# Kernel optimization log

Hardware: AMD Instinct MI355X
Metric: run time of the kernel (lower is better)

## Reference

```python
import jax, jax.numpy as jnp
import numpy as np

N = 100000
MUL = 16


def _build_cg():
    # Real-basis Clebsch-Gordan (Wigner-3j-style) coefficients, shape (2l1+1, 2l2+1, 2lo+1),
    # each normalized to unit Frobenius norm per output component (e3nn component normalization).
    eps = np.zeros((3, 3, 3), np.float32)
    for a, b, c in [(0, 1, 2), (1, 2, 0), (2, 0, 1)]:
        eps[a, b, c] = 1.0
        eps[a, c, b] = -1.0
    s2 = np.float32(1.0 / np.sqrt(2.0))
    q = np.zeros((5, 3, 3), np.float32)  # l=2 real harmonics: xy, yz, 3z^2-r^2, xz, x^2-y^2
    q[0, 0, 1] = q[0, 1, 0] = s2
    q[1, 1, 2] = q[1, 2, 1] = s2
    q[2] = np.diag([-1.0, -1.0, 2.0]).astype(np.float32) / np.sqrt(6.0)
    q[3, 0, 2] = q[3, 2, 0] = s2
    q[4] = np.diag([1.0, -1.0, 0.0]).astype(np.float32) * s2
    cg000 = jnp.ones((1, 1, 1), jnp.float32)                                   # 0e x 0e -> 0e
    cg011 = jnp.asarray(np.eye(3, dtype=np.float32)[None])                      # 0e x 1o -> 1o
    cg110 = jnp.asarray((np.eye(3, dtype=np.float32) / np.sqrt(3.0))[:, :, None])  # 1o x 1o -> 0e
    cg111 = jnp.asarray(eps * s2)                                               # 1o x 1o -> 1e
    cg112 = jnp.asarray(np.transpose(q, (1, 2, 0)))                             # 1o x 1o -> 2e
    return cg000, cg011, cg110, cg111, cg112


def _path(x1, x2, cg, w, alpha):
    # 'uvw' tensor-product path: out[z,w,m] = alpha * sum_{u,v,i,j} x1[z,u,i] x2[z,v,j] cg[i,j,m] w[u,v,w]
    # Contraction order chosen to keep the largest intermediate at [z,u,w,j].
    t = jnp.einsum('zvj,uvw->zuwj', x2, w)
    s = jnp.einsum('zui,zuwj->zwij', x1, t)
    return alpha * jnp.einsum('zwij,ijm->zwm', s, cg)


def _tensor_square(x, w0, w1, w2, w3, w4):
    n = x.shape[0]
    x0 = x[:, :MUL].reshape(n, MUL, 1)       # 16x0e
    x1 = x[:, MUL:].reshape(n, MUL, 3)       # 16x1o
    cg000, cg011, cg110, cg111, cg112 = _build_cg()
    a2 = 1.0 / np.sqrt(MUL * MUL * 2.0)      # 0e output receives 2 paths
    a1 = 1.0 / np.sqrt(MUL * MUL * 1.0)
    o_0e = _path(x0, x0, cg000, w0, a2) + _path(x1, x1, cg110, w2, a2)
    o_1o = _path(x0, x1, cg011, w1, a1)
    o_1e = _path(x1, x1, cg111, w3, a1)
    o_2e = _path(x1, x1, cg112, w4, a1)
    return jnp.concatenate([o.reshape(n, -1) for o in (o_0e, o_1o, o_1e, o_2e)], axis=1)


def setup_inputs() -> dict:
    key = jax.random.key(0)
    kx, k0, k1, k2, k3, k4 = jax.random.split(key, 6)
    return {
        'x': jax.random.normal(kx, (N, MUL * 1 + MUL * 3), jnp.float32),
        'w0': jax.random.normal(k0, (MUL, MUL, MUL), jnp.float32),
        'w1': jax.random.normal(k1, (MUL, MUL, MUL), jnp.float32),
        'w2': jax.random.normal(k2, (MUL, MUL, MUL), jnp.float32),
        'w3': jax.random.normal(k3, (MUL, MUL, MUL), jnp.float32),
        'w4': jax.random.normal(k4, (MUL, MUL, MUL), jnp.float32),
    }


def reference(x, w0, w1, w2, w3, w4):
    return _tensor_square(x, w0, w1, w2, w3, w4)
```

## Files before the change

### kernel.cpp

```cpp
#include <hip/hip_runtime.h>
#include <hip/hip_bf16.h>

typedef __attribute__((ext_vector_type(8))) short short8;
typedef __attribute__((ext_vector_type(4))) float float4v;
typedef __attribute__((ext_vector_type(4))) int int4v;

#define S_A 0.04419417382415922f
#define S_B 0.025515518153991442f
#define S_C 0.0625f

static __device__ __forceinline__ unsigned short f2bfu(float f) {
    __hip_bfloat16 h = __float2bfloat16(f);
    return __builtin_bit_cast(unsigned short, h);
}

static __device__ __forceinline__ unsigned pack_bf2(float a, float b) {
    return ((unsigned)f2bfu(b) << 16) | (unsigned)f2bfu(a);
}

__global__ __launch_bounds__(256, 2)
void tsq_kernel(const float* __restrict__ x,
                const float* __restrict__ wA,
                const float* __restrict__ wB,
                const float* __restrict__ wC,
                const float* __restrict__ wD,
                const float* __restrict__ wE,
                float* __restrict__ out,
                int nrows)
{
    __shared__ __attribute__((aligned(16))) unsigned short wlds[5 * 8 * 64 * 8];
    __shared__ __attribute__((aligned(16))) float xlds[64 * 68];

    const int tid = threadIdx.x;

    #pragma unroll
    for (int p = 0; p < 5; p++) {
        const float* wp = (p == 0) ? wA : (p == 1) ? wB : (p == 2) ? wC : (p == 3) ? wD : wE;
        for (int rem = tid; rem < 4096; rem += 256) {
            int k = rem >> 4;
            int w = rem & 15;
            int c = k >> 5, kk = k & 31;
            int lane = ((kk >> 3) << 4) | w;
            int j = kk & 7;
            wlds[(((p * 8 + c) * 64 + lane) << 3) | j] = f2bfu(wp[rem]);
        }
    }

    {
        const long long rowbase = (long long)blockIdx.x * 64;
        const float* xg = x + rowbase * 64;
        #pragma unroll
        for (int q = 0; q < 4; q++) {
            int f = q * 1024 + tid * 4;
            int row = f >> 6, col = f & 63;
            float4v v = {0.f, 0.f, 0.f, 0.f};
            if (rowbase + row < nrows) v = *(const float4v*)(xg + f);
            *(float4v*)&xlds[row * 68 + col] = v;
        }
    }
    __syncthreads();

    const int wave = tid >> 6;
    const int l = tid & 63;
    const long long z0 = (long long)blockIdx.x * 64 + wave * 16;
    if (z0 >= nrows) return;

    const int r  = l & 15;
    const int g  = l >> 4;
    const int v0 = (g & 1) * 8;
    const int uo = g >> 1;
    const float* xr = &xlds[(wave * 16 + r) * 68];

    float av[8], bx[8], byv[8], bzv[8];
    #pragma unroll
    for (int j = 0; j < 8; j++) {
        av[j]  = xr[v0 + j];
        bx[j]  = xr[16 + (v0 + j) * 3 + 0];
        byv[j] = xr[16 + (v0 + j) * 3 + 1];
        bzv[j] = xr[16 + (v0 + j) * 3 + 2];
    }

    float4v acc[13];
    #pragma unroll
    for (int m = 0; m < 13; m++) acc[m] = (float4v){0.f, 0.f, 0.f, 0.f};

    constexpr int pm[13] = {0, 1, 2, 2, 2, 3, 3, 3, 4, 4, 4, 4, 4};

    #pragma unroll
    for (int c = 0; c < 8; c++) {
        const int u = c * 2 + uo;
        const float u0 = xr[u];
        const float ux = xr[16 + u * 3 + 0];
        const float uy = xr[16 + u * 3 + 1];
        const float uz = xr[16 + u * 3 + 2];

        int4v fri[13];
        #pragma unroll
        for (int t = 0; t < 4; t++) {
            float bva[13], bvb[13];
            auto build = [&](int j, float* bv) {
                const float A0 = av[j], X = bx[j], Y = byv[j], Z = bzv[j];
                const float p00 = ux * X, p01 = ux * Y, p02 = ux * Z;
                const float p10 = uy * X, p11 = uy * Y, p12 = uy * Z;
                const float p20 = uz * X, p21 = uz * Y, p22 = uz * Z;
                bv[0]  = u0 * A0;
                bv[1]  = p00 + p11 + p22;
                bv[2]  = u0 * X;
                bv[3]  = u0 * Y;
                bv[4]  = u0 * Z;
                bv[5]  = p12 - p21;
                bv[6]  = p20 - p02;
                bv[7]  = p01 - p10;
                bv[8]  = p01 + p10;
                bv[9]  = p12 + p21;
                bv[10] = 2.0f * p22 - p00 - p11;
                bv[11] = p02 + p20;
                bv[12] = p00 - p11;
            };
            build(2 * t, bva);
            build(2 * t + 1, bvb);
            #pragma unroll
            for (int m = 0; m < 13; m++) fri[m][t] = (int)pack_bf2(bva[m], bvb[m]);
        }

        short8 wf[5];
        #pragma unroll
        for (int p = 0; p < 5; p++)
            wf[p] = *(const short8*)&wlds[(((p * 8 + c) * 64 + l) << 3)];

        #pragma unroll
        for (int m = 0; m < 13; m++) {
            short8 frm = __builtin_bit_cast(short8, fri[m]);
            acc[m] = __builtin_amdgcn_mfma_f32_16x16x32_bf16(frm, wf[pm[m]], acc[m], 0, 0, 0);
        }
    }

    const int w = r;
    float* outp = out + (z0 + g * 4) * 192;
    #pragma unroll
    for (int reg = 0; reg < 4; reg++) {
        float* rowp = outp + reg * 192;
        rowp[w] = S_A * acc[0][reg] + S_B * acc[1][reg];
        rowp[16 + w * 3 + 0]  = S_C * acc[2][reg];
        rowp[16 + w * 3 + 1]  = S_C * acc[3][reg];
        rowp[16 + w * 3 + 2]  = S_C * acc[4][reg];
        rowp[64 + w * 3 + 0]  = S_A * acc[5][reg];
        rowp[64 + w * 3 + 1]  = S_A * acc[6][reg];
        rowp[64 + w * 3 + 2]  = S_A * acc[7][reg];
        rowp[112 + w * 5 + 0] = S_A * acc[8][reg];
        rowp[112 + w * 5 + 1] = S_A * acc[9][reg];
        rowp[112 + w * 5 + 2] = S_B * acc[10][reg];
        rowp[112 + w * 5 + 3] = S_A * acc[11][reg];
        rowp[112 + w * 5 + 4] = S_A * acc[12][reg];
    }
}

extern "C" void kernel_launch(void* const* d_in, const int* in_sizes, int n_in,
                              void* d_out, int out_size, void* d_ws, size_t ws_size,
                              hipStream_t stream) {
    const float* x  = (const float*)d_in[0];
    const float* w0 = (const float*)d_in[1];
    const float* w1 = (const float*)d_in[2];
    const float* w2 = (const float*)d_in[3];
    const float* w3 = (const float*)d_in[4];
    const float* w4 = (const float*)d_in[5];
    float* out = (float*)d_out;
    (void)d_ws; (void)ws_size; (void)n_in;

    const int nrows = in_sizes[0] / 64;
    const int nblocks = (nrows + 63) / 64;
    tsq_kernel<<<dim3(nblocks), dim3(256), 0, stream>>>(x, w0, w2, w1, w3, w4, out, nrows);
}
```

Before: 145.1 us.

## Precompute bf16 weight fragments in a prep kernel and read them from global

Adds a small prep kernel that converts the five weight tensors to bf16 MFMA fragment layout once into workspace. The main kernel then loads fragments straight from global/L2 instead of every block rebuilding a 40KB LDS copy. With LDS down to the x tile, occupancy is raised to 4 blocks per CU. It also vectorizes the x loads from LDS, computes the pair products as float2, and uses a packed bf16 convert. This adds a second launch and per-iteration global loads in the inner loop.

Result: slower. 190.3 us (+31.1%).

```diff
diff --git a/kernel.cpp b/kernel.cpp
--- a/kernel.cpp
+++ b/kernel.cpp
@@ -3,48 +3,52 @@
 
 typedef __attribute__((ext_vector_type(8))) short short8;
 typedef __attribute__((ext_vector_type(4))) float float4v;
-typedef __attribute__((ext_vector_type(4))) int int4v;
+typedef __attribute__((ext_vector_type(2))) float float2v;
 
 #define S_A 0.04419417382415922f
 #define S_B 0.025515518153991442f
 #define S_C 0.0625f
 
-static __device__ __forceinline__ unsigned short f2bfu(float f) {
-    __hip_bfloat16 h = __float2bfloat16(f);
-    return __builtin_bit_cast(unsigned short, h);
+static __device__ __forceinline__ unsigned pkbf(float a, float b) {
+#if __has_builtin(__builtin_amdgcn_cvt_pk_bf16_f32)
+    auto v = __builtin_amdgcn_cvt_pk_bf16_f32(a, b);
+    return __builtin_bit_cast(unsigned, v);
+#else
+    unsigned ua = __builtin_bit_cast(unsigned, a);
+    unsigned ub = __builtin_bit_cast(unsigned, b);
+    ua += 0x7fffu + ((ua >> 16) & 1u);
+    ub += 0x7fffu + ((ub >> 16) & 1u);
+    return __builtin_amdgcn_perm(ub, ua, 0x07060302);
+#endif
 }
 
-static __device__ __forceinline__ unsigned pack_bf2(float a, float b) {
-    return ((unsigned)f2bfu(b) << 16) | (unsigned)f2bfu(a);
+__global__ void wprep_kernel(const float* __restrict__ wA, const float* __restrict__ wB,
+                             const float* __restrict__ wC, const float* __restrict__ wD,
+                             const float* __restrict__ wE, unsigned short* __restrict__ wout)
+{
+    int e = blockIdx.x * 256 + threadIdx.x;
+    if (e >= 5 * 4096) return;
+    int p = e >> 12;
+    int rem = e & 4095;
+    const float* wp = (p == 0) ? wA : (p == 1) ? wB : (p == 2) ? wC : (p == 3) ? wD : wE;
+    unsigned u = __builtin_bit_cast(unsigned, wp[rem]);
+    u += 0x7fffu + ((u >> 16) & 1u);
+    int k = rem >> 4, w = rem & 15;
+    int c = k >> 5, kk = k & 31;
+    int lane = ((kk >> 3) << 4) | w;
+    int j = kk & 7;
+    wout[(((c * 5 + p) * 64 + lane) << 3) | j] = (unsigned short)(u >> 16);
 }
 
-__global__ __launch_bounds__(256, 2)
+__global__ __launch_bounds__(256, 4)
 void tsq_kernel(const float* __restrict__ x,
-                const float* __restrict__ wA,
-                const float* __restrict__ wB,
-                const float* __restrict__ wC,
-                const float* __restrict__ wD,
-                const float* __restrict__ wE,
+                const unsigned short* __restrict__ wfrag,
                 float* __restrict__ out,
                 int nrows)
 {
-    __shared__ __attribute__((aligned(16))) unsigned short wlds[5 * 8 * 64 * 8];
     __shared__ __attribute__((aligned(16))) float xlds[64 * 68];
 
     const int tid = threadIdx.x;
-
-    #pragma unroll
-    for (int p = 0; p < 5; p++) {
-        const float* wp = (p == 0) ? wA : (p == 1) ? wB : (p == 2) ? wC : (p == 3) ? wD : wE;
-        for (int rem = tid; rem < 4096; rem += 256) {
-            int k = rem >> 4;
-            int w = rem & 15;
-            int c = k >> 5, kk = k & 31;
-            int lane = ((kk >> 3) << 4) | w;
-            int j = kk & 7;
-            wlds[(((p * 8 + c) * 64 + lane) << 3) | j] = f2bfu(wp[rem]);
-        }
-    }
 
     {
         const long long rowbase = (long long)blockIdx.x * 64;
@@ -71,13 +75,20 @@
     const int uo = g >> 1;
     const float* xr = &xlds[(wave * 16 + r) * 68];
 
-    float av[8], bx[8], byv[8], bzv[8];
-    #pragma unroll
-    for (int j = 0; j < 8; j++) {
-        av[j]  = xr[v0 + j];
-        bx[j]  = xr[16 + (v0 + j) * 3 + 0];
-        byv[j] = xr[16 + (v0 + j) * 3 + 1];
-        bzv[j] = xr[16 + (v0 + j) * 3 + 2];
+    float2v A0v[4], Xv[4], Yv[4], Zv[4];
+    {
+        float a[8], b[24];
+        #pragma unroll
+        for (int q = 0; q < 2; q++) *(float4v*)&a[q * 4] = *(const float4v*)(xr + v0 + q * 4);
+        #pragma unroll
+        for (int q = 0; q < 6; q++) *(float4v*)&b[q * 4] = *(const float4v*)(xr + 16 + v0 * 3 + q * 4);
+        #pragma unroll
+        for (int t = 0; t < 4; t++) {
+            A0v[t] = (float2v){a[2 * t], a[2 * t + 1]};
+            Xv[t]  = (float2v){b[6 * t + 0], b[6 * t + 3]};
+            Yv[t]  = (float2v){b[6 * t + 1], b[6 * t + 4]};
+            Zv[t]  = (float2v){b[6 * t + 2], b[6 * t + 5]};
+        }
     }
 
     float4v acc[13];
@@ -86,51 +97,48 @@
 
     constexpr int pm[13] = {0, 1, 2, 2, 2, 3, 3, 3, 4, 4, 4, 4, 4};
 
+    const short8* wbase = (const short8*)wfrag;
+
     #pragma unroll
     for (int c = 0; c < 8; c++) {
+        short8 wf[5];
+        #pragma unroll
+        for (int p = 0; p < 5; p++) wf[p] = wbase[(c * 5 + p) * 64 + l];
+
         const int u = c * 2 + uo;
         const float u0 = xr[u];
         const float ux = xr[16 + u * 3 + 0];
         const float uy = xr[16 + u * 3 + 1];
         const float uz = xr[16 + u * 3 + 2];
 
-        int4v fri[13];
+        unsigned fri[13][4];
         #pragma unroll
         for (int t = 0; t < 4; t++) {
-            float bva[13], bvb[13];
-            auto build = [&](int j, float* bv) {
-                const float A0 = av[j], X = bx[j], Y = byv[j], Z = bzv[j];
-                const float p00 = ux * X, p01 = ux * Y, p02 = ux * Z;
-                const float p10 = uy * X, p11 = uy * Y, p12 = uy * Z;
-                const float p20 = uz * X, p21 = uz * Y, p22 = uz * Z;
-                bv[0]  = u0 * A0;
-                bv[1]  = p00 + p11 + p22;
-                bv[2]  = u0 * X;
-                bv[3]  = u0 * Y;
-                bv[4]  = u0 * Z;
-                bv[5]  = p12 - p21;
-                bv[6]  = p20 - p02;
-                bv[7]  = p01 - p10;
-                bv[8]  = p01 + p10;
-                bv[9]  = p12 + p21;
-                bv[10] = 2.0f * p22 - p00 - p11;
-                bv[11] = p02 + p20;
-                bv[12] = p00 - p11;
-            };
-            build(2 * t, bva);
-            build(2 * t + 1, bvb);
+            const float2v X = Xv[t], Y = Yv[t], Z = Zv[t];
+            const float2v p00 = ux * X, p01 = ux * Y, p02 = ux * Z;
+            const float2v p10 = uy * X, p11 = uy * Y, p12 = uy * Z;
+            const float2v p20 = uz * X, p21 = uz * Y, p22 = uz * Z;
+            float2v bv[13];
+            bv[0]  = u0 * A0v[t];
+            bv[1]  = p00 + p11 + p22;
+            bv[2]  = u0 * X;
+            bv[3]  = u0 * Y;
+            bv[4]  = u0 * Z;
+            bv[5]  = p12 - p21;
+            bv[6]  = p20 - p02;
+            bv[7]  = p01 - p10;
+            bv[8]  = p01 + p10;
+            bv[9]  = p12 + p21;
+            bv[10] = 2.0f * p22 - p00 - p11;
+            bv[11] = p02 + p20;
+            bv[12] = p00 - p11;
             #pragma unroll
-            for (int m = 0; m < 13; m++) fri[m][t] = (int)pack_bf2(bva[m], bvb[m]);
+            for (int m = 0; m < 13; m++) fri[m][t] = pkbf(bv[m].x, bv[m].y);
         }
-
-        short8 wf[5];
-        #pragma unroll
-        for (int p = 0; p < 5; p++)
-            wf[p] = *(const short8*)&wlds[(((p * 8 + c) * 64 + l) << 3)];
 
         #pragma unroll
         for (int m = 0; m < 13; m++) {
-            short8 frm = __builtin_bit_cast(short8, fri[m]);
+            short8 frm = __builtin_bit_cast(short8, *(unsigned __attribute__((ext_vector_type(4)))*)fri[m]);
             acc[m] = __builtin_amdgcn_mfma_f32_16x16x32_bf16(frm, wf[pm[m]], acc[m], 0, 0, 0);
         }
     }
@@ -165,9 +173,12 @@
     const float* w3 = (const float*)d_in[4];
     const float* w4 = (const float*)d_in[5];
     float* out = (float*)d_out;
-    (void)d_ws; (void)ws_size; (void)n_in;
+    unsigned short* wfrag = (unsigned short*)d_ws;
+    (void)ws_size; (void)n_in; (void)out_size;
 
     const int nrows = in_sizes[0] / 64;
     const int nblocks = (nrows + 63) / 64;
-    tsq_kernel<<<dim3(nblocks), dim3(256), 0, stream>>>(x, w0, w2, w1, w3, w4, out, nrows);
+
+    wprep_kernel<<<dim3(80), dim3(256), 0, stream>>>(w0, w2, w1, w3, w4, wfrag);
+    tsq_kernel<<<dim3(nblocks), dim3(256), 0, stream>>>(x, wfrag, out, nrows);
 }
```
